# Optimization experiments

Measured on AMD Instinct MI355X. Metric: run time of the kernel, lower is better.

The kernel has to match this reference:

```python
import jax, jax.numpy as jnp
import numpy as np

EMBED = 1024
HEADS = 16
HEAD_DIM = EMBED // HEADS
HIDDEN = 4096
EPS = 1e-6


def _layer_norm(x, gamma, beta):
    mu = jnp.mean(x, axis=-1, keepdims=True)
    var = jnp.mean(jnp.square(x - mu), axis=-1, keepdims=True)
    return (x - mu) * jax.lax.rsqrt(var + EPS) * gamma + beta


def setup_inputs() -> dict:
    key = jax.random.key(0)
    ks = jax.random.split(key, 16)
    s = 1.0 / np.sqrt(EMBED)
    sh = 1.0 / np.sqrt(HIDDEN)
    return {
        "x": jax.random.normal(ks[0], (2, 2048, EMBED), dtype=jnp.float32),
        "Wq": jax.random.uniform(ks[1], (EMBED, EMBED), jnp.float32, -s, s),
        "bq": jnp.zeros((EMBED,), jnp.float32),
        "Wk": jax.random.uniform(ks[2], (EMBED, EMBED), jnp.float32, -s, s),
        "bk": jnp.zeros((EMBED,), jnp.float32),
        "Wv": jax.random.uniform(ks[3], (EMBED, EMBED), jnp.float32, -s, s),
        "bv": jnp.zeros((EMBED,), jnp.float32),
        "Wo": jax.random.uniform(ks[4], (EMBED, EMBED), jnp.float32, -s, s),
        "bo": jnp.zeros((EMBED,), jnp.float32),
        "ln1_g": jnp.ones((EMBED,), jnp.float32),
        "ln1_b": jnp.zeros((EMBED,), jnp.float32),
        "W1": jax.random.uniform(ks[5], (EMBED, HIDDEN), jnp.float32, -s, s),
        "b1": jnp.zeros((HIDDEN,), jnp.float32),
        "W2": jax.random.uniform(ks[6], (HIDDEN, EMBED), jnp.float32, -sh, sh),
        "b2": jnp.zeros((EMBED,), jnp.float32),
        "ln2_g": jnp.ones((EMBED,), jnp.float32),
        "ln2_b": jnp.zeros((EMBED,), jnp.float32),
    }


def reference(x, Wq, bq, Wk, bk, Wv, bv, Wo, bo, ln1_g, ln1_b, W1, b1, W2, b2, ln2_g, ln2_b):
    B, S, _ = x.shape
    # projections (weights stored as [in, out])
    q = (x @ Wq + bq).reshape(B, S, HEADS, HEAD_DIM)
    k = (x @ Wk + bk).reshape(B, S, HEADS, HEAD_DIM)
    v = (x @ Wv + bv).reshape(B, S, HEADS, HEAD_DIM)
    # scores: [B, H, S, S]
    scores = jnp.einsum('bqhd,bkhd->bhqk', q, k) / jnp.sqrt(jnp.float32(HEAD_DIM))
    attn = jax.nn.softmax(scores, axis=-1)
    ctx = jnp.einsum('bhqk,bkhd->bqhd', attn, v).reshape(B, S, EMBED)
    attn_out = ctx @ Wo + bo
    x1 = _layer_norm(x + attn_out, ln1_g, ln1_b)
    ffn = jax.nn.relu(x1 @ W1 + b1) @ W2 + b2
    return _layer_norm(x1 + ffn, ln2_g, ln2_b)
```

## Files before the change

kernel.cpp:

```cpp
#include <hip/hip_runtime.h>
#include <math.h>

#define EMBED 1024
#define HEADS 16
#define HDIM  64
#define HIDDEN 4096
#define BATCH 2
#define SEQ   2048
#define TOK   (BATCH * SEQ)

typedef _Float16 f16;
typedef f16 f16x8 __attribute__((ext_vector_type(8)));
typedef f16 f16x4 __attribute__((ext_vector_type(4)));
typedef float f32x4 __attribute__((ext_vector_type(4)));
typedef float f32x16 __attribute__((ext_vector_type(16)));

__device__ __forceinline__ void gload16(const void* g, void* s) {
  __builtin_amdgcn_global_load_lds(
      (const __attribute__((address_space(1))) unsigned int*)g,
      (__attribute__((address_space(3))) unsigned int*)s, 16, 0, 0);
}

template<int A16, int RELU, int OUT16, int QKV, int SPLITK>
__global__ __launch_bounds__(256, 3)
void gemm_f16(const void* __restrict__ Av, const f16* __restrict__ Wt,
              const float* __restrict__ bias0, const float* __restrict__ bias1,
              const float* __restrict__ bias2, void* __restrict__ Cv,
              int N, int K, int nbx) {
  __shared__ f16 As[512 * 8];
  __shared__ f16 Bs[512 * 8];
  const int tid = threadIdx.x;
  const int l = tid & 63, w = tid >> 6;
  const int g = l >> 4, ln = l & 15;
  int bid = blockIdx.x;
  int slice = 0;
  if (SPLITK > 1) { slice = bid % SPLITK; bid /= SPLITK; }
  const int ntiles = gridDim.x / SPLITK;
  const int cpx = ntiles >> 3;
  bid = (bid & 7) * cpx + (bid >> 3);
  const int m0 = (bid / nbx) << 7;
  const int n0 = (bid % nbx) << 7;
  const int wr = w >> 1, wc = w & 1;
  const int ksl = K / SPLITK;
  const int kbeg = slice * ksl, kend = kbeg + ksl;

  f32x4 acc[4][4] = {};

  for (int k0 = kbeg; k0 < kend; k0 += 32) {
    if (A16) {
      const f16* A = (const f16*)Av;
#pragma unroll
      for (int p = 0; p < 2; ++p) {
        const int u0 = p * 256 + w * 64;
        const int ks = u0 >> 7;
        const int row = ((u0 + l) & 127) ^ ks;
        gload16(A + (size_t)(m0 + row) * K + k0 + ks * 8, (void*)&As[u0 * 8]);
      }
    } else {
      const float* A = (const float*)Av;
      const int ks = tid & 3;
      const int r0 = tid >> 2;
#pragma unroll
      for (int p = 0; p < 2; ++p) {
        const int row = r0 + p * 64;
        const float* src = A + (size_t)(m0 + row) * K + k0 + ks * 8;
        float4 f0 = *(const float4*)src;
        float4 f1 = *(const float4*)(src + 4);
        f16x8 hh;
        hh[0] = (f16)f0.x; hh[1] = (f16)f0.y; hh[2] = (f16)f0.z; hh[3] = (f16)f0.w;
        hh[4] = (f16)f1.x; hh[5] = (f16)f1.y; hh[6] = (f16)f1.z; hh[7] = (f16)f1.w;
        *(f16x8*)&As[(ks * 128 + (row ^ ks)) * 8] = hh;
      }
    }
#pragma unroll
    for (int p = 0; p < 2; ++p) {
      const int u0 = p * 256 + w * 64;
      const int ks = u0 >> 7;
      const int col = ((u0 + l) & 127) ^ ks;
      gload16(Wt + (size_t)(n0 + col) * K + k0 + ks * 8, (void*)&Bs[u0 * 8]);
    }
    __syncthreads();
    f16x8 af[4], bf[4];
#pragma unroll
    for (int m = 0; m < 4; ++m)
      af[m] = *(const f16x8*)&As[(g * 128 + ((wr * 64 + m * 16 + ln) ^ g)) * 8];
#pragma unroll
    for (int n = 0; n < 4; ++n)
      bf[n] = *(const f16x8*)&Bs[(g * 128 + ((wc * 64 + n * 16 + ln) ^ g)) * 8];
#pragma unroll
    for (int m = 0; m < 4; ++m)
#pragma unroll
      for (int n = 0; n < 4; ++n)
        acc[m][n] = __builtin_amdgcn_mfma_f32_16x16x32_f16(af[m], bf[n], acc[m][n], 0, 0, 0);
    __syncthreads();
  }

  if (SPLITK > 1) {
    float* P = (float*)Cv + (size_t)slice * TOK * N;
#pragma unroll
    for (int m = 0; m < 4; ++m)
#pragma unroll
      for (int n = 0; n < 4; ++n)
#pragma unroll
        for (int r = 0; r < 4; ++r) {
          const size_t idx = (size_t)(m0 + wr * 64 + m * 16 + g * 4 + r) * N
                           + n0 + wc * 64 + n * 16 + ln;
          P[idx] = acc[m][n][r];
        }
    return;
  }

  const float* bp = bias0;
  int nbase = n0;
  float scale = 1.f;
  if (QKV) {
    const int seg = n0 >> 10;
    bp = (seg == 0) ? bias0 : (seg == 1) ? bias1 : bias2;
    nbase = n0 & 1023;
    if (seg == 0) scale = 0.125f * 1.44269504f;
  }
  float bv[4];
#pragma unroll
  for (int n = 0; n < 4; ++n) bv[n] = bp[nbase + wc * 64 + n * 16 + ln];
#pragma unroll
  for (int m = 0; m < 4; ++m)
#pragma unroll
    for (int n = 0; n < 4; ++n)
#pragma unroll
      for (int r = 0; r < 4; ++r) {
        float v = (acc[m][n][r] + bv[n]) * scale;
        if (RELU) v = fmaxf(v, 0.f);
        const size_t idx = (size_t)(m0 + wr * 64 + m * 16 + g * 4 + r) * N
                         + n0 + wc * 64 + n * 16 + ln;
        if (OUT16) ((f16*)Cv)[idx] = (f16)v;
        else       ((float*)Cv)[idx] = v;
      }
}

template<int BASE>
__device__ __forceinline__ f16x8 pack_frag(f32x16 p) {
  f16x8 r;
#pragma unroll
  for (int j = 0; j < 8; ++j) r[j] = (f16)p[BASE + j];
  return r;
}

#define VSTRIDE 68
#define NKT (SEQ / 64)

__global__ __launch_bounds__(256, 2)
void attention(const f16* __restrict__ qkv, f16* __restrict__ ctx) {
  __shared__ f16 Ks[2][64 * 64];
  __shared__ f16 VTs[2][64 * VSTRIDE];
  const int tid = threadIdx.x;
  const int l = tid & 63, w = tid >> 6;
  const int ln = l & 31, hi = l >> 5;
  const int bh = blockIdx.y, b = bh >> 4, h = bh & 15;
  const int q0 = blockIdx.x * 128;

  f16x8 qf[4];
  {
    const f16* qp = qkv + (size_t)(b * SEQ + q0 + w * 32 + ln) * 3072 + h * 64 + hi * 8;
#pragma unroll
    for (int kc = 0; kc < 4; ++kc) qf[kc] = *(const f16x8*)(qp + kc * 16);
  }

  f32x16 o0 = {}, o1 = {};
  float mrow = -1e30f, lrow = 0.f;

  const int skey = tid >> 3, sc = tid & 7;
  const f16* kbase = qkv + (size_t)(b * SEQ) * 3072 + 1024 + h * 64;
  const f16* vbase = qkv + (size_t)(b * SEQ) * 3072 + 2048 + h * 64;
  const int wbase = sc * 8 * VSTRIDE + (skey ^ (sc << 2));

  auto gloadK = [&](int buf, int kt) {
#pragma unroll
    for (int p = 0; p < 2; ++p) {
      const int key = p * 32 + skey;
      gload16(kbase + (size_t)(kt * 64 + key) * 3072 + 8 * (sc ^ (key & 7)),
              (void*)&Ks[buf][(p * 256 + w * 64) * 8]);
    }
  };
  auto scatterV = [&](int buf, f16x8 va, f16x8 vb2) {
#pragma unroll
    for (int j = 0; j < 8; ++j) {
      VTs[buf][wbase + VSTRIDE * j] = va[j];
      VTs[buf][wbase + VSTRIDE * j + 32] = vb2[j];
    }
  };

  {
    const f16* vp = vbase + (size_t)skey * 3072 + sc * 8;
    f16x8 va = *(const f16x8*)vp;
    f16x8 vb2 = *(const f16x8*)(vp + (size_t)32 * 3072);
    gloadK(0, 0);
    scatterV(0, va, vb2);
  }
  __syncthreads();

  const int sw0 = (ln >> 3) << 2;
  const int db0 = ln * VSTRIDE, db1 = (32 + ln) * VSTRIDE;

  auto body = [&](int kt, int cur) {
    const int nxt = cur ^ 1;
    f16x8 vna = {}, vnb = {};
    const bool more = (kt + 1 < NKT);
    if (more) {
      const f16* vp = vbase + (size_t)((kt + 1) * 64 + skey) * 3072 + sc * 8;
      vna = *(const f16x8*)vp;
      vnb = *(const f16x8*)(vp + (size_t)32 * 3072);
      gloadK(nxt, kt + 1);
    }
    f32x16 st0 = {}, st1 = {};
    __builtin_amdgcn_s_setprio(1);
#pragma unroll
    for (int kc = 0; kc < 4; ++kc) {
      const int m = kc * 2 + hi;
      const f16x8 kf0 = *(const f16x8*)&Ks[cur][(ln * 8 + (m ^ (ln & 7))) * 8];
      const f16x8 kf1 = *(const f16x8*)&Ks[cur][((32 + ln) * 8 + (m ^ (ln & 7))) * 8];
      st0 = __builtin_amdgcn_mfma_f32_32x32x16_f16(kf0, qf[kc], st0, 0, 0, 0);
      st1 = __builtin_amdgcn_mfma_f32_32x32x16_f16(kf1, qf[kc], st1, 0, 0, 0);
    }
    __builtin_amdgcn_s_setprio(0);

    float tm[16];
#pragma unroll
    for (int r = 0; r < 16; ++r) tm[r] = fmaxf(st0[r], st1[r]);
#pragma unroll
    for (int s2 = 8; s2 >= 1; s2 >>= 1)
#pragma unroll
      for (int r = 0; r < s2; ++r) tm[r] = fmaxf(tm[r], tm[r + s2]);
    const float mt = fmaxf(tm[0], __shfl_xor(tm[0], 32));
    if (!__all(mt <= mrow + 8.f)) {
      const float mn = fmaxf(mrow, mt);
      const float al = exp2f(mrow - mn);
      mrow = mn;
      lrow *= al;
#pragma unroll
      for (int r = 0; r < 16; ++r) { o0[r] *= al; o1[r] *= al; }
    }
    float ts[16];
#pragma unroll
    for (int r = 0; r < 16; ++r) {
      st0[r] = exp2f(st0[r] - mrow);
      st1[r] = exp2f(st1[r] - mrow);
      ts[r] = st0[r] + st1[r];
    }
#pragma unroll
    for (int s2 = 8; s2 >= 1; s2 >>= 1)
#pragma unroll
      for (int r = 0; r < s2; ++r) ts[r] += ts[r + s2];
    lrow += ts[0] + __shfl_xor(ts[0], 32);

    f16x8 pf[4];
    pf[0] = pack_frag<0>(st0); pf[1] = pack_frag<8>(st0);
    pf[2] = pack_frag<0>(st1); pf[3] = pack_frag<8>(st1);

    __builtin_amdgcn_s_setprio(1);
#pragma unroll
    for (int s = 0; s < 4; ++s) {
      const int k0 = 16 * s + 4 * hi;
      {
        const int p0 = k0 ^ sw0;
        f16x4 x = *(const f16x4*)&VTs[cur][db0 + p0];
        f16x4 y = *(const f16x4*)&VTs[cur][db0 + (p0 ^ 8)];
        f16x8 vf = __builtin_shufflevector(x, y, 0, 1, 2, 3, 4, 5, 6, 7);
        o0 = __builtin_amdgcn_mfma_f32_32x32x16_f16(vf, pf[s], o0, 0, 0, 0);
      }
      {
        const int p1 = k0 ^ sw0 ^ 16;
        f16x4 x = *(const f16x4*)&VTs[cur][db1 + p1];
        f16x4 y = *(const f16x4*)&VTs[cur][db1 + (p1 ^ 8)];
        f16x8 vf = __builtin_shufflevector(x, y, 0, 1, 2, 3, 4, 5, 6, 7);
        o1 = __builtin_amdgcn_mfma_f32_32x32x16_f16(vf, pf[s], o1, 0, 0, 0);
      }
    }
    __builtin_amdgcn_s_setprio(0);

    if (more) scatterV(nxt, vna, vnb);
    __syncthreads();
  };

#pragma unroll 1
  for (int kt = 0; kt < NKT; kt += 2) { body(kt, 0); body(kt + 1, 1); }

  const float inv = 1.f / lrow;
  f16* cp = ctx + (size_t)(b * SEQ + q0 + w * 32 + ln) * EMBED + h * 64;
#pragma unroll
  for (int r = 0; r < 16; ++r) {
    const int drow = (r & 3) + 8 * (r >> 2) + 4 * hi;
    cp[drow] = (f16)(o0[r] * inv);
    cp[32 + drow] = (f16)(o1[r] * inv);
  }
}

template<int NP, int OUT16>
__global__ __launch_bounds__(256, 4)
void add_ln(const float* parts, const float* __restrict__ bias,
            const float* resid, const float* __restrict__ gam,
            const float* __restrict__ bet, float* out, f16* __restrict__ out16) {
  const int t = blockIdx.x;
  const int tid = threadIdx.x;
  const size_t base = (size_t)t * EMBED + tid * 4;
  float4 rv = *(const float4*)(resid + base);
  float4 bb = *(const float4*)(bias + tid * 4);
  float x0 = rv.x + bb.x, x1 = rv.y + bb.y, x2 = rv.z + bb.z, x3 = rv.w + bb.w;
#pragma unroll
  for (int p = 0; p < NP; ++p) {
    float4 pv = *(const float4*)(parts + (size_t)p * TOK * EMBED + base);
    x0 += pv.x; x1 += pv.y; x2 += pv.z; x3 += pv.w;
  }
  float s1 = x0 + x1 + x2 + x3;
  float s2 = x0 * x0 + x1 * x1 + x2 * x2 + x3 * x3;
  for (int off = 1; off < 64; off <<= 1) {
    s1 += __shfl_xor(s1, off);
    s2 += __shfl_xor(s2, off);
  }
  __shared__ float red[8];
  if ((tid & 63) == 0) { red[(tid >> 6) * 2] = s1; red[(tid >> 6) * 2 + 1] = s2; }
  __syncthreads();
  s1 = red[0] + red[2] + red[4] + red[6];
  s2 = red[1] + red[3] + red[5] + red[7];
  const float mu = s1 * (1.f / EMBED);
  const float var = s2 * (1.f / EMBED) - mu * mu;
  const float rstd = rsqrtf(var + 1e-6f);
  float4 gv = *(const float4*)(gam + tid * 4);
  float4 bv = *(const float4*)(bet + tid * 4);
  float4 ov;
  ov.x = (x0 - mu) * rstd * gv.x + bv.x;
  ov.y = (x1 - mu) * rstd * gv.y + bv.y;
  ov.z = (x2 - mu) * rstd * gv.z + bv.z;
  ov.w = (x3 - mu) * rstd * gv.w + bv.w;
  *(float4*)(out + base) = ov;
  if (OUT16) {
    f16x4 hh;
    hh[0] = (f16)ov.x; hh[1] = (f16)ov.y; hh[2] = (f16)ov.z; hh[3] = (f16)ov.w;
    *(f16x4*)(out16 + base) = hh;
  }
}

__device__ __forceinline__ void transpose_tile(const float* in, f16* out,
                                               int K, int N, int k0, int n0, int tid) {
  __shared__ float t[32][33];
  {
    const int ky = tid >> 3, nx = (tid & 7) * 4;
    float4 f = *(const float4*)(in + (size_t)(k0 + ky) * N + n0 + nx);
    t[ky][nx] = f.x; t[ky][nx + 1] = f.y; t[ky][nx + 2] = f.z; t[ky][nx + 3] = f.w;
  }
  __syncthreads();
  const int ny = tid >> 3, kx = (tid & 7) * 4;
  f16x4 hh;
  hh[0] = (f16)t[kx][ny];     hh[1] = (f16)t[kx + 1][ny];
  hh[2] = (f16)t[kx + 2][ny]; hh[3] = (f16)t[kx + 3][ny];
  *(f16x4*)(out + (size_t)(n0 + ny) * K + k0 + kx) = hh;
}

__global__ __launch_bounds__(256, 4)
void transpose_w(const float* __restrict__ in, f16* __restrict__ out,
                 int K, int N) {
  transpose_tile(in, out, K, N, blockIdx.y * 32, blockIdx.x * 32, threadIdx.x);
}

__global__ __launch_bounds__(256, 4)
void transpose_qkv(const float* __restrict__ w0, const float* __restrict__ w1,
                   const float* __restrict__ w2, f16* __restrict__ out) {
  const float* in = (blockIdx.z == 0) ? w0 : (blockIdx.z == 1) ? w1 : w2;
  f16* o = out + (size_t)blockIdx.z * 1024 * 1024;
  transpose_tile(in, o, 1024, 1024, blockIdx.y * 32, blockIdx.x * 32, threadIdx.x);
}

extern "C" void kernel_launch(void* const* d_in, const int* in_sizes, int n_in,
                              void* d_out, int out_size, void* d_ws, size_t ws_size,
                              hipStream_t stream) {
  const float* x    = (const float*)d_in[0];
  const float* Wq   = (const float*)d_in[1];
  const float* bq   = (const float*)d_in[2];
  const float* Wk   = (const float*)d_in[3];
  const float* bk   = (const float*)d_in[4];
  const float* Wv   = (const float*)d_in[5];
  const float* bv   = (const float*)d_in[6];
  const float* Wo   = (const float*)d_in[7];
  const float* bo   = (const float*)d_in[8];
  const float* ln1g = (const float*)d_in[9];
  const float* ln1b = (const float*)d_in[10];
  const float* W1   = (const float*)d_in[11];
  const float* b1   = (const float*)d_in[12];
  const float* W2   = (const float*)d_in[13];
  const float* b2   = (const float*)d_in[14];
  const float* ln2g = (const float*)d_in[15];
  const float* ln2b = (const float*)d_in[16];
  float* out = (float*)d_out;

  char* ws = (char*)d_ws;
  const size_t MB = 1024 * 1024;
  f16*   WtQKV = (f16*)(ws);
  f16*   WtO   = (f16*)(ws + 6 * MB);
  f16*   Wt1   = (f16*)(ws + 8 * MB);
  f16*   Wt2   = (f16*)(ws + 16 * MB);
  f16*   qkv   = (f16*)(ws + 24 * MB);
  f16*   ctx   = (f16*)(ws + 48 * MB);
  float* parts = (float*)(ws + 56 * MB);
  f16*   x1h   = (f16*)(ws + 88 * MB);
  f16*   hid   = (f16*)(ws + 24 * MB);
  float* x1    = out;

  const dim3 blk(256);
  transpose_qkv<<<dim3(32, 32, 3), blk, 0, stream>>>(Wq, Wk, Wv, WtQKV);
  transpose_w<<<dim3(32, 32), blk, 0, stream>>>(Wo, WtO, 1024, 1024);
  transpose_w<<<dim3(128, 32), blk, 0, stream>>>(W1, Wt1, 1024, 4096);
  transpose_w<<<dim3(32, 128), blk, 0, stream>>>(W2, Wt2, 4096, 1024);

  gemm_f16<0, 0, 1, 1, 1><<<768, blk, 0, stream>>>(x, WtQKV, bq, bk, bv, qkv, 3072, 1024, 24);
  attention<<<dim3(16, 32), blk, 0, stream>>>(qkv, ctx);
  gemm_f16<1, 0, 0, 0, 2><<<512, blk, 0, stream>>>(ctx, WtO, nullptr, nullptr, nullptr, parts, 1024, 1024, 8);
  add_ln<2, 1><<<4096, blk, 0, stream>>>(parts, bo, x, ln1g, ln1b, x1, x1h);
  gemm_f16<1, 1, 1, 0, 1><<<1024, blk, 0, stream>>>(x1h, Wt1, b1, nullptr, nullptr, hid, 4096, 1024, 32);
  gemm_f16<1, 0, 0, 0, 2><<<512, blk, 0, stream>>>(hid, Wt2, nullptr, nullptr, nullptr, parts, 1024, 4096, 8);
  add_ln<2, 0><<<4096, blk, 0, stream>>>(parts, b2, x1, ln2g, ln2b, out, nullptr);
}
```

Baseline: 448.1 us.

## Double-buffer GEMM LDS tiles and pre-cast x to f16 for async loads

The GEMM kernel now keeps two LDS buffers for A and B. It prefetches the tile two steps ahead with global_load_lds while MFMAs run on the current tile, and uses explicit vmcnt waits, raw barriers and setprio around the MFMA block. To make every GEMM use the async f16 path, a separate cast kernel converts x to f16 up front, which removes the fp32-A template path. The cost is double the LDS per block, which may cut occupancy at launch bounds of 3, plus an extra kernel launch and one more pass over x in memory.

```diff
diff --git a/kernel.cpp b/kernel.cpp
--- a/kernel.cpp
+++ b/kernel.cpp
@@ -21,14 +21,14 @@
       (__attribute__((address_space(3))) unsigned int*)s, 16, 0, 0);
 }
 
-template<int A16, int RELU, int OUT16, int QKV, int SPLITK>
+template<int RELU, int OUT16, int QKV, int SPLITK>
 __global__ __launch_bounds__(256, 3)
-void gemm_f16(const void* __restrict__ Av, const f16* __restrict__ Wt,
+void gemm_f16(const f16* __restrict__ A, const f16* __restrict__ Wt,
               const float* __restrict__ bias0, const float* __restrict__ bias1,
               const float* __restrict__ bias2, void* __restrict__ Cv,
               int N, int K, int nbx) {
-  __shared__ f16 As[512 * 8];
-  __shared__ f16 Bs[512 * 8];
+  __shared__ f16 As[2][512 * 8];
+  __shared__ f16 Bs[2][512 * 8];
   const int tid = threadIdx.x;
   const int l = tid & 63, w = tid >> 6;
   const int g = l >> 4, ln = l & 15;
@@ -46,53 +46,56 @@
 
   f32x4 acc[4][4] = {};
 
-  for (int k0 = kbeg; k0 < kend; k0 += 32) {
-    if (A16) {
-      const f16* A = (const f16*)Av;
-#pragma unroll
-      for (int p = 0; p < 2; ++p) {
-        const int u0 = p * 256 + w * 64;
-        const int ks = u0 >> 7;
-        const int row = ((u0 + l) & 127) ^ ks;
-        gload16(A + (size_t)(m0 + row) * K + k0 + ks * 8, (void*)&As[u0 * 8]);
-      }
-    } else {
-      const float* A = (const float*)Av;
-      const int ks = tid & 3;
-      const int r0 = tid >> 2;
-#pragma unroll
-      for (int p = 0; p < 2; ++p) {
-        const int row = r0 + p * 64;
-        const float* src = A + (size_t)(m0 + row) * K + k0 + ks * 8;
-        float4 f0 = *(const float4*)src;
-        float4 f1 = *(const float4*)(src + 4);
-        f16x8 hh;
-        hh[0] = (f16)f0.x; hh[1] = (f16)f0.y; hh[2] = (f16)f0.z; hh[3] = (f16)f0.w;
-        hh[4] = (f16)f1.x; hh[5] = (f16)f1.y; hh[6] = (f16)f1.z; hh[7] = (f16)f1.w;
-        *(f16x8*)&As[(ks * 128 + (row ^ ks)) * 8] = hh;
-      }
+  auto stage = [&](int buf, int k0) {
+#pragma unroll
+    for (int p = 0; p < 2; ++p) {
+      const int u0 = p * 256 + w * 64;
+      const int ks = u0 >> 7;
+      const int row = ((u0 + l) & 127) ^ ks;
+      gload16(A + (size_t)(m0 + row) * K + k0 + ks * 8, (void*)&As[buf][u0 * 8]);
     }
 #pragma unroll
     for (int p = 0; p < 2; ++p) {
       const int u0 = p * 256 + w * 64;
       const int ks = u0 >> 7;
       const int col = ((u0 + l) & 127) ^ ks;
-      gload16(Wt + (size_t)(n0 + col) * K + k0 + ks * 8, (void*)&Bs[u0 * 8]);
-    }
-    __syncthreads();
+      gload16(Wt + (size_t)(n0 + col) * K + k0 + ks * 8, (void*)&Bs[buf][u0 * 8]);
+    }
+  };
+
+  stage(0, kbeg);
+  stage(1, kbeg + 32);
+  asm volatile("s_waitcnt vmcnt(4)" ::: "memory");
+  __builtin_amdgcn_s_barrier();
+
+  int cur = 0;
+#pragma unroll 1
+  for (int k0 = kbeg; k0 < kend; k0 += 32) {
     f16x8 af[4], bf[4];
 #pragma unroll
     for (int m = 0; m < 4; ++m)
-      af[m] = *(const f16x8*)&As[(g * 128 + ((wr * 64 + m * 16 + ln) ^ g)) * 8];
+      af[m] = *(const f16x8*)&As[cur][(g * 128 + ((wr * 64 + m * 16 + ln) ^ g)) * 8];
 #pragma unroll
     for (int n = 0; n < 4; ++n)
-      bf[n] = *(const f16x8*)&Bs[(g * 128 + ((wc * 64 + n * 16 + ln) ^ g)) * 8];
+      bf[n] = *(const f16x8*)&Bs[cur][(g * 128 + ((wc * 64 + n * 16 + ln) ^ g)) * 8];
+    asm volatile("s_waitcnt lgkmcnt(0)" ::: "memory");
+    __builtin_amdgcn_sched_barrier(0);
+    __builtin_amdgcn_s_barrier();
+    const bool morestage = (k0 + 64 < kend);
+    if (morestage) stage(cur, k0 + 64);
+    __builtin_amdgcn_s_setprio(1);
 #pragma unroll
     for (int m = 0; m < 4; ++m)
 #pragma unroll
       for (int n = 0; n < 4; ++n)
         acc[m][n] = __builtin_amdgcn_mfma_f32_16x16x32_f16(af[m], bf[n], acc[m][n], 0, 0, 0);
-    __syncthreads();
+    __builtin_amdgcn_s_setprio(0);
+    if (k0 + 32 < kend) {
+      if (morestage) asm volatile("s_waitcnt vmcnt(4)" ::: "memory");
+      else           asm volatile("s_waitcnt vmcnt(0)" ::: "memory");
+      __builtin_amdgcn_s_barrier();
+    }
+    cur ^= 1;
   }
 
   if (SPLITK > 1) {
@@ -135,6 +138,15 @@
         if (OUT16) ((f16*)Cv)[idx] = (f16)v;
         else       ((float*)Cv)[idx] = v;
       }
+}
+
+__global__ __launch_bounds__(256, 4)
+void cast_f16(const float* __restrict__ in, f16* __restrict__ out) {
+  const size_t i = ((size_t)blockIdx.x * 256 + threadIdx.x) * 4;
+  float4 f = *(const float4*)(in + i);
+  f16x4 hh;
+  hh[0] = (f16)f.x; hh[1] = (f16)f.y; hh[2] = (f16)f.z; hh[3] = (f16)f.w;
+  *(f16x4*)(out + i) = hh;
 }
 
 template<int BASE>
@@ -399,6 +411,7 @@
   f16*   Wt2   = (f16*)(ws + 16 * MB);
   f16*   qkv   = (f16*)(ws + 24 * MB);
   f16*   ctx   = (f16*)(ws + 48 * MB);
+  f16*   x16   = (f16*)(ws + 48 * MB);
   float* parts = (float*)(ws + 56 * MB);
   f16*   x1h   = (f16*)(ws + 88 * MB);
   f16*   hid   = (f16*)(ws + 24 * MB);
@@ -409,12 +422,13 @@
   transpose_w<<<dim3(32, 32), blk, 0, stream>>>(Wo, WtO, 1024, 1024);
   transpose_w<<<dim3(128, 32), blk, 0, stream>>>(W1, Wt1, 1024, 4096);
   transpose_w<<<dim3(32, 128), blk, 0, stream>>>(W2, Wt2, 4096, 1024);
-
-  gemm_f16<0, 0, 1, 1, 1><<<768, blk, 0, stream>>>(x, WtQKV, bq, bk, bv, qkv, 3072, 1024, 24);
+  cast_f16<<<4096, blk, 0, stream>>>(x, x16);
+
+  gemm_f16<0, 1, 1, 1><<<768, blk, 0, stream>>>(x16, WtQKV, bq, bk, bv, qkv, 3072, 1024, 24);
   attention<<<dim3(16, 32), blk, 0, stream>>>(qkv, ctx);
-  gemm_f16<1, 0, 0, 0, 2><<<512, blk, 0, stream>>>(ctx, WtO, nullptr, nullptr, nullptr, parts, 1024, 1024, 8);
+  gemm_f16<0, 0, 0, 2><<<512, blk, 0, stream>>>(ctx, WtO, nullptr, nullptr, nullptr, parts, 1024, 1024, 8);
   add_ln<2, 1><<<4096, blk, 0, stream>>>(parts, bo, x, ln1g, ln1b, x1, x1h);
-  gemm_f16<1, 1, 1, 0, 1><<<1024, blk, 0, stream>>>(x1h, Wt1, b1, nullptr, nullptr, hid, 4096, 1024, 32);
-  gemm_f16<1, 0, 0, 0, 2><<<512, blk, 0, stream>>>(hid, Wt2, nullptr, nullptr, nullptr, parts, 1024, 4096, 8);
+  gemm_f16<1, 1, 0, 1><<<1024, blk, 0, stream>>>(x1h, Wt1, b1, nullptr, nullptr, hid, 4096, 1024, 32);
+  gemm_f16<0, 0, 0, 2><<<512, blk, 0, stream>>>(hid, Wt2, nullptr, nullptr, nullptr, parts, 1024, 4096, 8);
   add_ln<2, 0><<<4096, blk, 0, stream>>>(parts, b2, x1, ln2g, ln2b, out, nullptr);
 }
```

Result: no change. 448.5 us (+0.1%).
